# Performance work log

Hardware: AMD Instinct MI355X
Metric: run time of the kernel (lower is better)

The kernel has to match this reference:

```python
import jax, jax.numpy as jnp
import numpy as np

N, E = 50000, 800000
IN, MAP, H, O = 256, 64, 4, 64
LEAKY_SLOPE = 0.2


def setup_inputs() -> dict:
    key = jax.random.key(0)
    ks = jax.random.split(key, 12)
    x = jax.random.normal(ks[0], (N, IN), dtype=jnp.float32)
    src = jax.random.randint(ks[1], (E,), 0, N, dtype=jnp.int32)
    dst = jax.random.randint(ks[2], (E,), 0, N, dtype=jnp.int32)
    s = 1.0 / np.sqrt(IN)
    W_gat = jax.random.normal(ks[3], (IN, H * O), dtype=jnp.float32) * s
    attn_l = jax.random.normal(ks[4], (H, O), dtype=jnp.float32) * 0.1
    attn_r = jax.random.normal(ks[5], (H, O), dtype=jnp.float32) * 0.1
    gate_m_W = jax.random.normal(ks[6], (IN, MAP), dtype=jnp.float32) * s
    gate_m_b = jnp.zeros((MAP,), dtype=jnp.float32)
    gate_fn_W = jax.random.normal(ks[7], (2 * IN + MAP, H), dtype=jnp.float32) * (1.0 / np.sqrt(2 * IN + MAP))
    gate_fn_b = jnp.zeros((H,), dtype=jnp.float32)
    merge_W = jax.random.normal(ks[8], (IN + O, O), dtype=jnp.float32) * (1.0 / np.sqrt(IN + O))
    merge_b = jnp.zeros((O,), dtype=jnp.float32)
    return {"x": x, "src": src, "dst": dst, "W_gat": W_gat, "attn_l": attn_l,
            "attn_r": attn_r, "gate_m_W": gate_m_W, "gate_m_b": gate_m_b,
            "gate_fn_W": gate_fn_W, "gate_fn_b": gate_fn_b,
            "merge_W": merge_W, "merge_b": merge_b}


def _forward(x, src, dst, W_gat, attn_l, attn_r, gate_m_W, gate_m_b,
             gate_fn_W, gate_fn_b, merge_W, merge_b):
    n = x.shape[0]
    # --- gate branch: gspmm mean of x, gspmm max of linear_z over in-neighbors ---
    deg = jax.ops.segment_sum(jnp.ones_like(dst, dtype=x.dtype), dst, num_segments=n)
    mean_z = jax.ops.segment_sum(x[src], dst, num_segments=n) / jnp.maximum(deg, 1.0)[:, None]
    z = x @ gate_m_W + gate_m_b  # [N, MAP]
    max_z = jax.ops.segment_max(z[src], dst, num_segments=n)
    max_z = jnp.where(deg[:, None] > 0, max_z, 0.0)  # empty neighborhoods -> 0
    nft = jnp.concatenate([x, max_z, mean_z], axis=1)  # [N, 2*IN+MAP]
    gate = jax.nn.sigmoid(nft @ gate_fn_W + gate_fn_b)  # [N, H]
    # --- GATConv ---
    feat = (x @ W_gat).reshape(n, H, O)  # [N, H, O]
    el = jnp.einsum('nho,ho->nh', feat, attn_l)
    er = jnp.einsum('nho,ho->nh', feat, attn_r)
    e = jax.nn.leaky_relu(el[src] + er[dst], negative_slope=LEAKY_SLOPE)  # [E, H]
    m = jax.ops.segment_max(e, dst, num_segments=n)  # [N, H]
    m = jnp.where(jnp.isfinite(m), m, 0.0)
    ex = jnp.exp(e - m[dst])  # [E, H]
    s = jax.ops.segment_sum(ex, dst, num_segments=n)  # [N, H]
    alpha = ex / jnp.maximum(s[dst], 1e-16)  # [E, H]
    attn_out = jax.ops.segment_sum(feat[src] * alpha[:, :, None], dst, num_segments=n)  # [N, H, O]
    # --- gated merge ---
    gated = (gate[:, :, None] * attn_out).mean(axis=1)  # [N, O]
    merge = jnp.concatenate([x, gated], axis=1) @ merge_W + merge_b  # [N, O]
    return merge


def reference(x, src, dst, W_gat, attn_l, attn_r, gate_m_W, gate_m_b,
              gate_fn_W, gate_fn_b, merge_W, merge_b):
    return _forward(x, src, dst, W_gat, attn_l, attn_r, gate_m_W, gate_m_b,
                    gate_fn_W, gate_fn_b, merge_W, merge_b)
```

## Files before the change

### kernel.cpp

```cpp
#include <hip/hip_runtime.h>
#include <math.h>

#define NN 50000
#define NE 800000
#define LEAKY 0.2f
#define NT 26
#define CAP 96
#define NBT (8 * NT * 64)
#define BT_BLKS 54

typedef short bf16x8 __attribute__((ext_vector_type(8)));
typedef float f32x4 __attribute__((ext_vector_type(4)));
typedef float f32x2 __attribute__((ext_vector_type(2)));

__device__ __forceinline__ unsigned short f2bf(float f) {
  unsigned u = __float_as_uint(f);
  u += 0x7fffu + ((u >> 16) & 1u);
  return (unsigned short)(u >> 16);
}
__device__ __forceinline__ float leaky(float v) { return v > 0.0f ? v : LEAKY * v; }
__device__ __forceinline__ float rlf(float v, int l) {
  return __uint_as_float(__builtin_amdgcn_readlane(__float_as_uint(v), l));
}
__device__ __forceinline__ int rli(int v, int l) {
  return __builtin_amdgcn_readlane(v, l);
}

__device__ __forceinline__ bf16x8 ld_a_bf16(const float* p) {
  float4 fa = *(const float4*)p;
  float4 fb = *(const float4*)(p + 4);
  unsigned r0, r1, r2, r3;
  asm("v_cvt_pk_bf16_f32 %0, %1, %2" : "=v"(r0) : "v"(fa.x), "v"(fa.y));
  asm("v_cvt_pk_bf16_f32 %0, %1, %2" : "=v"(r1) : "v"(fa.z), "v"(fa.w));
  asm("v_cvt_pk_bf16_f32 %0, %1, %2" : "=v"(r2) : "v"(fb.x), "v"(fb.y));
  asm("v_cvt_pk_bf16_f32 %0, %1, %2" : "=v"(r3) : "v"(fb.z), "v"(fb.w));
  union { uint4 u; bf16x8 v; } c;
  c.u = make_uint4(r0, r1, r2, r3);
  return c.v;
}

#if defined(__has_builtin)
#if __has_builtin(__builtin_amdgcn_cvt_pk_f32_fp8) && \
    __has_builtin(__builtin_amdgcn_cvt_pk_fp8_f32) && \
    __has_builtin(__builtin_amdgcn_cvt_f32_fp8)
#define FP8_HW 1
#endif
#endif

#ifdef FP8_HW
__device__ __forceinline__ unsigned char f2fp8(float v) {
  return (unsigned char)(__builtin_amdgcn_cvt_pk_fp8_f32(v, v, 0u, false) & 0xFF);
}
__device__ __forceinline__ f32x2 fp8x2_lo(unsigned int v) {
  return __builtin_amdgcn_cvt_pk_f32_fp8(v, false);
}
__device__ __forceinline__ f32x2 fp8x2_hi(unsigned int v) {
  return __builtin_amdgcn_cvt_pk_f32_fp8(v, true);
}
__device__ __forceinline__ float fp8one(unsigned int v) {
  return __builtin_amdgcn_cvt_f32_fp8(v, 0);
}
#else
__device__ __forceinline__ unsigned char f2fp8(float f) {
  unsigned u = __float_as_uint(f);
  unsigned s = (u >> 31) << 7;
  unsigned a = u & 0x7FFFFFFFu;
  if (a >= 0x43E00000u) return (unsigned char)(s | 0x7E);
  if (a < 0x3C800000u) {
    float m = __uint_as_float(a) * 512.0f;
    int q = (int)(m + 0.5f); if (q > 7) q = 7;
    return (unsigned char)(s | q);
  }
  a += 0x7FFFFu + ((a >> 20) & 1);
  unsigned e = ((a >> 23) & 0xFF) - 120;
  if (e > 15) return (unsigned char)(s | 0x7E);
  return (unsigned char)(s | (e << 3) | ((a >> 20) & 7));
}
__device__ __forceinline__ float fp8dec1(unsigned b) {
  unsigned s = (b & 0x80u) << 24;
  unsigned em = b & 0x7Fu;
  unsigned e4 = em >> 3, m3 = em & 7;
  float v = e4 ? __uint_as_float(((e4 + 120) << 23) | (m3 << 20))
               : (float)m3 * 0.001953125f;
  return __uint_as_float(__float_as_uint(v) ^ s);
}
__device__ __forceinline__ f32x2 fp8x2_lo(unsigned int v) {
  f32x2 r; r[0] = fp8dec1(v & 0xFF); r[1] = fp8dec1((v >> 8) & 0xFF); return r;
}
__device__ __forceinline__ f32x2 fp8x2_hi(unsigned int v) {
  f32x2 r; r[0] = fp8dec1((v >> 16) & 0xFF); r[1] = fp8dec1((v >> 24) & 0xFF); return r;
}
__device__ __forceinline__ float fp8one(unsigned int v) { return fp8dec1(v & 0xFF); }
#endif

__device__ __forceinline__ float panel_w(int col, int k,
    const float* W_gat, const float* gate_m_W, const float* merge_W,
    const float* gate_fn_W) {
  if (col < 256)      return W_gat[k * 256 + (col & 3) * 64 + (col >> 2)];
  else if (col < 320) return gate_m_W[k * 64 + (col - 256)];
  else if (col < 384) return merge_W[k * 64 + (col - 320)];
  else if (col < 388) return gate_fn_W[k * 4 + (col - 384)];
  else if (col < 392) return gate_fn_W[(320 + k) * 4 + (col - 388)];
  return 0.0f;
}

__global__ __launch_bounds__(256) void k_prep(
    const float* __restrict__ W_gat, const float* __restrict__ gate_m_W,
    const float* __restrict__ merge_W, const float* __restrict__ gate_fn_W,
    unsigned short* __restrict__ Btf, unsigned short* __restrict__ mWf,
    unsigned char* __restrict__ zq, float* __restrict__ epay,
    unsigned char* __restrict__ featq) {
  int b = blockIdx.x, tid = threadIdx.x;
  int idx = b * 256 + tid;
  if (idx < NBT) {
    int kq = idx / (NT * 64);
    int rem = idx - kq * (NT * 64);
    int t = rem >> 6, lane = rem & 63;
    int col = t * 16 + (lane & 15);
    int k = kq * 32 + (lane >> 4) * 8;
    unsigned short* o = Btf + (size_t)idx * 8;
#pragma unroll
    for (int i = 0; i < 8; ++i)
      o[i] = f2bf(panel_w(col, k + i, W_gat, gate_m_W, merge_W, gate_fn_W));
  } else if (idx < NBT + 512) {
    int idx2 = idx - NBT;
    int kq = idx2 >> 8;
    int rem = idx2 & 255;
    int t = rem >> 6, lane = rem & 63;
    int col = t * 16 + (lane & 15);
    int k = kq * 32 + ((lane >> 4) & 3) * 8;
    unsigned short* o = mWf + (size_t)idx2 * 8;
#pragma unroll
    for (int i = 0; i < 8; ++i)
      o[i] = f2bf(merge_W[(size_t)(256 + k + i) * 64 + col]);
  } else if (b == BT_BLKS) {
    if (tid < 64) zq[(size_t)NN * 64 + tid] = 0xFE;
    if (tid < 8) epay[(size_t)NN * 8 + tid] = 0.0f;
    featq[(size_t)NN * 256 + tid] = 0;
  }
}

__global__ void k_scatter(const int* __restrict__ src, const int* __restrict__ dst,
                          int* __restrict__ cursor, unsigned short* __restrict__ csr_src) {
  int e = blockIdx.x * 256 + threadIdx.x;
  if (e < NE) {
    int n = dst[e];
    int pos = atomicAdd(&cursor[n], 1);
    if (pos < CAP) csr_src[n * CAP + pos] = (unsigned short)src[e];
  }
}

__global__ __launch_bounds__(256, 2) void k_gemm_mfma(
    const float* __restrict__ x, const unsigned short* __restrict__ Btf,
    const float* __restrict__ gate_m_b,
    const float* __restrict__ attn_l, const float* __restrict__ attn_r,
    unsigned char* __restrict__ featq, unsigned char* __restrict__ zq,
    float* __restrict__ xm, float* __restrict__ gx, float* __restrict__ epay,
    float* __restrict__ erv) {
  __shared__ float els[64][4][2];
  __shared__ float ers[64][4][2];
  int lane = threadIdx.x & 63;
  int wave = threadIdx.x >> 6;
  int rowHalf = wave >> 1, colHalf = wave & 1;
  int rowB = blockIdx.x * 64;
  int row0 = rowB + rowHalf * 32;
  int t0 = colHalf * 13;
  int m = lane & 15, kg = lane >> 4;
  f32x4 zero = {0.f, 0.f, 0.f, 0.f};
  f32x4 acc[2][13];
#pragma unroll
  for (int g = 0; g < 2; ++g)
#pragma unroll
    for (int t = 0; t < 13; ++t) acc[g][t] = zero;

  int r0i = row0 + m;
  int r1i = r0i + 16;
  if (r0i >= NN) r0i = NN - 1;
  if (r1i >= NN) r1i = NN - 1;
  const float* aP0 = x + (size_t)r0i * 256 + kg * 8;
  const float* aP1 = x + (size_t)r1i * 256 + kg * 8;
  const unsigned short* bB = Btf + (size_t)(t0 * 64 + lane) * 8;

  bf16x8 aC0, aC1, aN0, aN1, bC[13], bN[13];
  aC0 = ld_a_bf16(aP0);
  aC1 = ld_a_bf16(aP1);
#pragma unroll
  for (int t = 0; t < 13; ++t)
    bC[t] = *(const bf16x8*)(bB + (size_t)t * 512);
#pragma unroll 1
  for (int kq = 0; kq < 8; kq += 2) {
    aN0 = ld_a_bf16(aP0 + (kq + 1) * 32);
    aN1 = ld_a_bf16(aP1 + (kq + 1) * 32);
#pragma unroll
    for (int t = 0; t < 13; ++t)
      bN[t] = *(const bf16x8*)(bB + ((size_t)(kq + 1) * NT + t) * 512);
#pragma unroll
    for (int t = 0; t < 13; ++t)
      acc[0][t] = __builtin_amdgcn_mfma_f32_16x16x32_bf16(aC0, bC[t], acc[0][t], 0, 0, 0);
#pragma unroll
    for (int t = 0; t < 13; ++t)
      acc[1][t] = __builtin_amdgcn_mfma_f32_16x16x32_bf16(aC1, bC[t], acc[1][t], 0, 0, 0);
    int kq2 = kq + 2 < 8 ? kq + 2 : 7;
    aC0 = ld_a_bf16(aP0 + kq2 * 32);
    aC1 = ld_a_bf16(aP1 + kq2 * 32);
#pragma unroll
    for (int t = 0; t < 13; ++t)
      bC[t] = *(const bf16x8*)(bB + ((size_t)kq2 * NT + t) * 512);
#pragma unroll
    for (int t = 0; t < 13; ++t)
      acc[0][t] = __builtin_amdgcn_mfma_f32_16x16x32_bf16(aN0, bN[t], acc[0][t], 0, 0, 0);
#pragma unroll
    for (int t = 0; t < 13; ++t)
      acc[1][t] = __builtin_amdgcn_mfma_f32_16x16x32_bf16(aN1, bN[t], acc[1][t], 0, 0, 0);
  }

  int h = m & 3, od = m >> 2;
  float elp[2][4] = {{0,0,0,0},{0,0,0,0}}, erp[2][4] = {{0,0,0,0},{0,0,0,0}};
#pragma unroll
  for (int t = 0; t < 13; ++t) {
    if ((t0 + t) * 16 < 256) {
      int o = (t0 + t) * 4 + od;
      float al = attn_l[h * 64 + o];
      float ar = attn_r[h * 64 + o];
#pragma unroll
      for (int g = 0; g < 2; ++g)
#pragma unroll
        for (int r = 0; r < 4; ++r) {
          elp[g][r] += acc[g][t][r] * al;
          erp[g][r] += acc[g][t][r] * ar;
        }
    }
  }
#pragma unroll
  for (int g = 0; g < 2; ++g)
#pragma unroll
    for (int r = 0; r < 4; ++r) {
      elp[g][r] += __shfl_xor(elp[g][r], 4, 64); elp[g][r] += __shfl_xor(elp[g][r], 8, 64);
      erp[g][r] += __shfl_xor(erp[g][r], 4, 64); erp[g][r] += __shfl_xor(erp[g][r], 8, 64);
    }
  if (m < 4) {
#pragma unroll
    for (int g = 0; g < 2; ++g)
#pragma unroll
      for (int r = 0; r < 4; ++r) {
        els[rowHalf * 32 + g * 16 + kg * 4 + r][m][colHalf] = elp[g][r];
        ers[rowHalf * 32 + g * 16 + kg * 4 + r][m][colHalf] = erp[g][r];
      }
  }

#pragma unroll
  for (int g = 0; g < 2; ++g) {
    if (colHalf == 0) {
#pragma unroll
      for (int r = 0; r < 4; ++r) {
        int row = row0 + g * 16 + kg * 4 + r;
        if (row >= NN) continue;
#pragma unroll
        for (int t = 0; t < 13; ++t)
          featq[(size_t)row * 256 + t * 16 + m] = f2fp8(acc[g][t][r]);
      }
    } else {
#pragma unroll
      for (int r = 0; r < 4; ++r) {
        int row = row0 + g * 16 + kg * 4 + r;
        if (row >= NN) continue;
#pragma unroll
        for (int t = 0; t < 3; ++t)
          featq[(size_t)row * 256 + 208 + t * 16 + m] = f2fp8(acc[g][t][r]);
#pragma unroll
        for (int t = 3; t < 7; ++t) {
          int cc = (t - 3) * 16 + m;
          zq[(size_t)row * 64 + cc] = f2fp8(acc[g][t][r] + gate_m_b[cc]);
        }
#pragma unroll
        for (int t = 7; t < 11; ++t)
          xm[(size_t)row * 64 + (t - 7) * 16 + m] = acc[g][t][r];
        if (m < 4) gx[(size_t)row * 4 + m] = acc[g][11][r];
        else if (m < 8) epay[(size_t)row * 8 + (m - 4) * 2 + 1] = acc[g][11][r];
      }
    }
  }
  __syncthreads();
  int tid = threadIdx.x;
  {
    int rr = tid >> 2, h2 = tid & 3;
    int row = rowB + rr;
    if (row < NN) {
      epay[(size_t)row * 8 + h2 * 2] = els[rr][h2][0] + els[rr][h2][1];
      erv[(size_t)row * 4 + h2] = ers[rr][h2][0] + ers[rr][h2][1];
    }
  }
}

__global__ __launch_bounds__(256) void k_node(
    const unsigned char* __restrict__ zq, const unsigned char* __restrict__ featq,
    const float* __restrict__ epay, const float* __restrict__ er,
    const float* __restrict__ gx,
    const int* __restrict__ cursor, const unsigned short* __restrict__ csr_src,
    const float* __restrict__ gate_fn_W, const float* __restrict__ gate_fn_b,
    const unsigned short* __restrict__ mWf, const float* __restrict__ xm,
    const float* __restrict__ merge_b, float* __restrict__ out, int nbase) {
  __shared__ float WzT[4][64];
  __shared__ float pbuf[4][16][4];
  __shared__ unsigned short gLDS[16][72];
  int tid = threadIdx.x;
  {
    int c = tid >> 2, h = tid & 3;
    WzT[h][c] = gate_fn_W[(256 + c) * 4 + h];
  }
  __syncthreads();

  int lane = tid & 63, wave = tid >> 6;
  int hh = lane >> 4, le = lane & 15;
  int rowbase = nbase + blockIdx.x * 16;
  int nodeBase = rowbase + wave * 4;
#pragma unroll 1
  for (int i = 0; i < 4; ++i) {
    int node = nodeBase + i;
    int deg = cursor[node]; if (deg > CAP) deg = CAP;
    float gated = 0.0f;
    if (deg > 0) {
      int rs = node * CAP, re = rs + deg;
      float er_h = er[(size_t)node * 4 + hh];
      f32x2 A01 = {0.f, 0.f}, A23 = {0.f, 0.f};
      float psum = 0, usum = 0;
      float mz = -INFINITY;
      int jj = rs + le;
      int s_l = (jj < re) ? (int)csr_src[jj] : NN;
#pragma unroll 1
      for (int j0 = rs; j0 < re; j0 += 16) {
        int jn = j0 + 16 + le;
        int s_nx = (jn < re) ? (int)csr_src[jn] : NN;
        bool valid = (j0 + le) < re;
        float2 eu = *(const float2*)(epay + ((size_t)(unsigned)s_l << 3) + hh * 2);
        float p = valid ? __expf(leaky(eu.x + er_h)) : 0.0f;
        psum += p;
        usum += eu.y;
        pbuf[wave][le][hh] = p;
        unsigned int fvr[16];
        unsigned int zvr[16];
#pragma unroll
        for (int e2 = 0; e2 < 16; ++e2) {
          int s = rli(s_l, e2);
          fvr[e2] = *(const unsigned int*)(featq + ((size_t)(unsigned)s << 8) + lane * 4);
        }
#pragma unroll
        for (int e2 = 0; e2 < 16; ++e2) {
          int s = rli(s_l, e2);
          zvr[e2] = zq[((size_t)(unsigned)s << 6) + lane];
        }
#pragma unroll
        for (int e2 = 0; e2 < 16; ++e2) {
          float4 pv = *(const float4*)pbuf[wave][e2];
          f32x2 p01 = {pv.x, pv.y};
          f32x2 p23 = {pv.z, pv.w};
          A01 += p01 * fp8x2_lo(fvr[e2]);
          A23 += p23 * fp8x2_hi(fvr[e2]);
          mz = fmaxf(mz, fp8one(zvr[e2]));
        }
        s_l = s_nx;
      }
#pragma unroll
      for (int off = 1; off < 16; off <<= 1) {
        psum += __shfl_xor(psum, off, 64);
        usum += __shfl_xor(usum, off, 64);
      }
      float s0 = rlf(psum, 0),  s1 = rlf(psum, 16);
      float s2 = rlf(psum, 32), s3 = rlf(psum, 48);
      float su0 = rlf(usum, 0),  su1 = rlf(usum, 16);
      float su2 = rlf(usum, 32), su3 = rlf(usum, 48);

      float g[4];
#pragma unroll
      for (int h = 0; h < 4; ++h) {
        float t = mz * WzT[h][lane];
#pragma unroll
        for (int off = 32; off; off >>= 1) t += __shfl_xor(t, off, 64);
        g[h] = t;
      }
      float inv_deg = 1.0f / (float)deg;
      float4 gx4 = *(const float4*)(gx + (size_t)node * 4);
      float g0 = 1.0f / (1.0f + __expf(-(g[0] + gx4.x + su0 * inv_deg + gate_fn_b[0])));
      float g1 = 1.0f / (1.0f + __expf(-(g[1] + gx4.y + su1 * inv_deg + gate_fn_b[1])));
      float g2 = 1.0f / (1.0f + __expf(-(g[2] + gx4.z + su2 * inv_deg + gate_fn_b[2])));
      float g3 = 1.0f / (1.0f + __expf(-(g[3] + gx4.w + su3 * inv_deg + gate_fn_b[3])));
      gated = 0.25f * (g0 * A01[0] / s0 + g1 * A01[1] / s1 +
                       g2 * A23[0] / s2 + g3 * A23[1] / s3);
    }
    gLDS[wave * 4 + i][lane] = f2bf(gated);
  }
  __syncthreads();

  int m = lane & 15, kg = lane >> 4;
  f32x4 acc = {0.f, 0.f, 0.f, 0.f};
#pragma unroll
  for (int kq = 0; kq < 2; ++kq) {
    bf16x8 a = *(const bf16x8*)(&gLDS[m][kq * 32 + kg * 8]);
    bf16x8 b = *(const bf16x8*)(mWf + (((size_t)kq * 4 + wave) * 64 + lane) * 8);
    acc = __builtin_amdgcn_mfma_f32_16x16x32_bf16(a, b, acc, 0, 0, 0);
  }
  int c = wave * 16 + m;
  float mb = merge_b[c];
#pragma unroll
  for (int r = 0; r < 4; ++r) {
    int row = rowbase + kg * 4 + r;
    out[(size_t)row * 64 + c] = acc[r] + xm[(size_t)row * 64 + c] + mb;
  }
}

extern "C" void kernel_launch(void* const* d_in, const int* in_sizes, int n_in,
                              void* d_out, int out_size, void* d_ws, size_t ws_size,
                              hipStream_t stream) {
  const float* x         = (const float*)d_in[0];
  const int*   src       = (const int*)d_in[1];
  const int*   dst       = (const int*)d_in[2];
  const float* W_gat     = (const float*)d_in[3];
  const float* attn_l    = (const float*)d_in[4];
  const float* attn_r    = (const float*)d_in[5];
  const float* gate_m_W  = (const float*)d_in[6];
  const float* gate_m_b  = (const float*)d_in[7];
  const float* gate_fn_W = (const float*)d_in[8];
  const float* gate_fn_b = (const float*)d_in[9];
  const float* merge_W   = (const float*)d_in[10];
  const float* merge_b   = (const float*)d_in[11];
  float* out = (float*)d_out;

  char* ws = (char*)d_ws;
  size_t off = 0;
  auto alloc = [&](size_t bytes) -> void* {
    off = (off + 255) & ~(size_t)255;
    void* p = ws + off;
    off += bytes;
    return p;
  };
  int* cursor    = (int*)alloc((size_t)NN * 4);
  unsigned short* csr_src = (unsigned short*)alloc((size_t)NN * CAP * 2);
  float* epay = (float*)alloc((size_t)(NN + 1) * 8 * 4);
  float* er   = (float*)alloc((size_t)NN * 4 * 4);
  float* gx   = (float*)alloc((size_t)NN * 4 * 4);
  float* xm   = (float*)alloc((size_t)NN * 64 * 4);
  unsigned char* zq    = (unsigned char*)alloc((size_t)(NN + 1) * 64);
  unsigned char* featq = (unsigned char*)alloc((size_t)(NN + 1) * 256);
  unsigned short* Btf    = (unsigned short*)alloc((size_t)NBT * 8 * 2);
  unsigned short* mWf    = (unsigned short*)alloc((size_t)512 * 8 * 2);

  hipMemsetAsync(cursor, 0, (size_t)NN * 4, stream);
  k_prep<<<BT_BLKS + 1, 256, 0, stream>>>(W_gat, gate_m_W, merge_W, gate_fn_W,
                                          Btf, mWf, zq, epay, featq);
  k_scatter<<<(NE + 255) / 256, 256, 0, stream>>>(src, dst, cursor, csr_src);
  k_gemm_mfma<<<(NN + 63) / 64, 256, 0, stream>>>(x, Btf, gate_m_b, attn_l, attn_r,
                                                  featq, zq, xm, gx, epay, er);
  const int HALF1 = 1563;
  const int HALF2 = (NN / 16) - HALF1;
  k_node<<<HALF1, 256, 0, stream>>>(zq, featq, epay, er, gx, cursor, csr_src,
                                    gate_fn_W, gate_fn_b, mWf, xm, merge_b, out, 0);
  k_node<<<HALF2, 256, 0, stream>>>(zq, featq, epay, er, gx, cursor, csr_src,
                                    gate_fn_W, gate_fn_b, mWf, xm, merge_b, out,
                                    HALF1 * 16);
}
```

Baseline: 273.1 us.

## Fuse edge scatter into GEMM kernel via interleaved blocks; merge node launches

Folds the edge CSR scatter into the feature GEMM kernel by interleaving one GEMM block with four scatter blocks per group of five. Scatter's atomic, memory-bound work can then overlap the MFMA-bound GEMM on the same GPU, and a launch is saved. The two half-size node kernel launches become a single launch. The risk is that scatter blocks inherit the GEMM kernel's launch bounds and register allocation, which may limit their occupancy, and that the mixed block types could unbalance scheduling.

```diff
diff --git a/kernel.cpp b/kernel.cpp
--- a/kernel.cpp
+++ b/kernel.cpp
@@ -8,6 +8,9 @@
 #define CAP 96
 #define NBT (8 * NT * 64)
 #define BT_BLKS 54
+#define GEMM_BLKS 782
+#define SCAT_BLKS 3125
+#define FUSE_BLKS 3907
 
 typedef short bf16x8 __attribute__((ext_vector_type(8)));
 typedef float f32x4 __attribute__((ext_vector_type(4)));
@@ -140,29 +143,32 @@
   }
 }
 
-__global__ void k_scatter(const int* __restrict__ src, const int* __restrict__ dst,
-                          int* __restrict__ cursor, unsigned short* __restrict__ csr_src) {
-  int e = blockIdx.x * 256 + threadIdx.x;
-  if (e < NE) {
-    int n = dst[e];
-    int pos = atomicAdd(&cursor[n], 1);
-    if (pos < CAP) csr_src[n * CAP + pos] = (unsigned short)src[e];
-  }
-}
-
-__global__ __launch_bounds__(256, 2) void k_gemm_mfma(
+__global__ __launch_bounds__(256, 2) void k_gemm_scatter(
     const float* __restrict__ x, const unsigned short* __restrict__ Btf,
     const float* __restrict__ gate_m_b,
     const float* __restrict__ attn_l, const float* __restrict__ attn_r,
     unsigned char* __restrict__ featq, unsigned char* __restrict__ zq,
     float* __restrict__ xm, float* __restrict__ gx, float* __restrict__ epay,
-    float* __restrict__ erv) {
+    float* __restrict__ erv,
+    const int* __restrict__ src, const int* __restrict__ dst,
+    int* __restrict__ cursor, unsigned short* __restrict__ csr_src) {
   __shared__ float els[64][4][2];
   __shared__ float ers[64][4][2];
+  int bq = blockIdx.x / 5, br = blockIdx.x % 5;
+  if (br != 0) {
+    int sIdx = bq * 4 + (br - 1);
+    int e = sIdx * 256 + threadIdx.x;
+    if (e < NE) {
+      int n = dst[e];
+      int pos = atomicAdd(&cursor[n], 1);
+      if (pos < CAP) csr_src[n * CAP + pos] = (unsigned short)src[e];
+    }
+    return;
+  }
   int lane = threadIdx.x & 63;
   int wave = threadIdx.x >> 6;
   int rowHalf = wave >> 1, colHalf = wave & 1;
-  int rowB = blockIdx.x * 64;
+  int rowB = bq * 64;
   int row0 = rowB + rowHalf * 32;
   int t0 = colHalf * 13;
   int m = lane & 15, kg = lane >> 4;
@@ -299,7 +305,7 @@
     const int* __restrict__ cursor, const unsigned short* __restrict__ csr_src,
     const float* __restrict__ gate_fn_W, const float* __restrict__ gate_fn_b,
     const unsigned short* __restrict__ mWf, const float* __restrict__ xm,
-    const float* __restrict__ merge_b, float* __restrict__ out, int nbase) {
+    const float* __restrict__ merge_b, float* __restrict__ out) {
   __shared__ float WzT[4][64];
   __shared__ float pbuf[4][16][4];
   __shared__ unsigned short gLDS[16][72];
@@ -312,7 +318,7 @@
 
   int lane = tid & 63, wave = tid >> 6;
   int hh = lane >> 4, le = lane & 15;
-  int rowbase = nbase + blockIdx.x * 16;
+  int rowbase = blockIdx.x * 16;
   int nodeBase = rowbase + wave * 4;
 #pragma unroll 1
   for (int i = 0; i < 4; ++i) {
@@ -447,14 +453,9 @@
   hipMemsetAsync(cursor, 0, (size_t)NN * 4, stream);
   k_prep<<<BT_BLKS + 1, 256, 0, stream>>>(W_gat, gate_m_W, merge_W, gate_fn_W,
                                           Btf, mWf, zq, epay, featq);
-  k_scatter<<<(NE + 255) / 256, 256, 0, stream>>>(src, dst, cursor, csr_src);
-  k_gemm_mfma<<<(NN + 63) / 64, 256, 0, stream>>>(x, Btf, gate_m_b, attn_l, attn_r,
-                                                  featq, zq, xm, gx, epay, er);
-  const int HALF1 = 1563;
-  const int HALF2 = (NN / 16) - HALF1;
-  k_node<<<HALF1, 256, 0, stream>>>(zq, featq, epay, er, gx, cursor, csr_src,
-                                    gate_fn_W, gate_fn_b, mWf, xm, merge_b, out, 0);
-  k_node<<<HALF2, 256, 0, stream>>>(zq, featq, epay, er, gx, cursor, csr_src,
-                                    gate_fn_W, gate_fn_b, mWf, xm, merge_b, out,
-                                    HALF1 * 16);
-}
+  k_gemm_scatter<<<FUSE_BLKS, 256, 0, stream>>>(x, Btf, gate_m_b, attn_l, attn_r,
+                                                featq, zq, xm, gx, epay, er,
+                                                src, dst, cursor, csr_src);
+  k_node<<<NN / 16, 256, 0, stream>>>(zq, featq, epay, er, gx, cursor, csr_src,
+                                      gate_fn_W, gate_fn_b, mWf, xm, merge_b, out);
+}
```

Result: faster. 244.7 us (-10.4%).
